# Kernel tuning notes

Hardware: AMD Instinct MI355X
Metric: run time of the kernel (lower is better)

The kernel has to match this reference:

```python
import jax, jax.numpy as jnp
import numpy as np

NUM_HEADS = 8  # config.num_heads


def setup_inputs() -> dict:
    key = jax.random.key(0)
    k0, k1, k2, k3, k4 = jax.random.split(key, 5)
    B, N, C, E = 32, 20000, 8, 512
    query_embeddings = jax.random.normal(k0, (B, E), dtype=jnp.float32)
    all_embeddings = jax.random.normal(k1, (N, E), dtype=jnp.float32)
    label_mask = jax.random.bernoulli(k2, 0.5, (N, C))  # bool multi-label mask
    # per-class MultiheadAttention q/k in-projection params (torch Linear convention: x @ W.T + b)
    Wq = jax.random.normal(k3, (C, E, E), dtype=jnp.float32) * 0.02
    Wk = jax.random.normal(k4, (C, E, E), dtype=jnp.float32) * 0.02
    bq = jnp.zeros((C, E), dtype=jnp.float32)
    bk = jnp.zeros((C, E), dtype=jnp.float32)
    return {
        "query_embeddings": query_embeddings,
        "all_embeddings": all_embeddings,
        "label_mask": label_mask,
        "Wq": Wq,
        "bq": bq,
        "Wk": Wk,
        "bk": bk,
        "n_samples": 5,
    }


def reference(query_embeddings, all_embeddings, label_mask, Wq, bq, Wk, bk, n_samples):
    """Vectorized-over-classes version of EmbeddingSelector.get_similar_samples.

    For each class c: q = query @ Wq[c].T + bq[c]; k_c over the class's database
    members; per-head scaled-dot softmax; attn weights averaged over heads
    (torch MHA need_weights default); top-k over class members. Non-members are
    masked to -inf before softmax, so they get weight 0 and (since every class
    has >> n_samples members) never enter the top-k -- identical math to the
    per-class gather loop, with global indices returned directly.
    """
    C, E, _ = Wq.shape
    H = NUM_HEADS
    dh = E // H
    B = query_embeddings.shape[0]
    N = all_embeddings.shape[0]

    # per-class projections (torch Linear: x @ W.T + b)
    q = jnp.einsum('be,cfe->cbf', query_embeddings, Wq) + bq[:, None, :]   # (C,B,E)
    k = jnp.einsum('ne,cfe->cnf', all_embeddings, Wk) + bk[:, None, :]     # (C,N,E)
    q = q.reshape(C, B, H, dh)
    k = k.reshape(C, N, H, dh)

    scale = 1.0 / jnp.sqrt(jnp.asarray(dh, q.dtype))
    scores = jnp.einsum('cbhd,cnhd->cbhn', q, k) * scale                   # (C,B,H,N)
    member = jnp.transpose(label_mask)[:, None, None, :]                   # (C,1,1,N)
    scores = jnp.where(member, scores, jnp.asarray(-1e9, scores.dtype))
    attn = jax.nn.softmax(scores, axis=-1).mean(axis=2)                    # (C,B,N) head-avg

    weights, indices = jax.lax.top_k(attn, n_samples)                      # (C,B,ns)
    result_weights = jnp.transpose(weights, (1, 0, 2))                     # (B,C,ns)
    result_indices = jnp.transpose(indices, (1, 0, 2)).astype(jnp.int32)   # (B,C,ns) global ids
    return result_indices, result_weights
```

## Files before the change

### kernel.cpp

```cpp
#include <hip/hip_runtime.h>
#include <math.h>

#define B_  32
#define N_  20000
#define C_  8
#define E_  512
#define H_  8
#define SCALE 0.125f
#define UNSC  9.765625e-4f

#define CHUNK 1024
#define NCH   20
#define NC3   157
#define NCG   20
#define SSZ ((size_t)B_ * H_ * N_)

typedef __attribute__((ext_vector_type(8))) _Float16 h8_t;
typedef __attribute__((ext_vector_type(8))) short   s8_t;
typedef __attribute__((ext_vector_type(4))) float f32x4;

#define MFMAH(a, b, c) __builtin_amdgcn_mfma_f32_16x16x32_f16(a, b, c, 0, 0, 0)

#define GLOAD_LDS16(g, l)                                              \
    __builtin_amdgcn_global_load_lds(                                  \
        (const __attribute__((address_space(1))) unsigned int*)(g),    \
        (__attribute__((address_space(3))) unsigned int*)(l), 16, 0, 0)

__device__ inline unsigned short f16_round(float x, float& fv) {
    _Float16 h = (_Float16)x;
    fv = (float)h;
    union { _Float16 hh; unsigned short us; } u;
    u.hh = h;
    return u.us;
}

#define U2P ((size_t)C_ * 16 * 16 * 512)

__global__ __launch_bounds__(256) void k_prep(
        const float* __restrict__ A, short* __restrict__ A2t,
        const float* __restrict__ x, const float* __restrict__ Wq,
        const float* __restrict__ bq, float* __restrict__ q) {
    int bid = blockIdx.x;
    int tid = threadIdx.x;
    if (bid < NC3 * 16) {
        int nc = bid >> 4, ks = bid & 15;
        int n = tid >> 1, kg = (tid & 1) * 2;
        int gn = nc * 128 + n;
        const float* ap = A + (size_t)gn * 512 + ks * 32 + kg * 8;
        s8_t vh[2], vm[2];
        #pragma unroll
        for (int g = 0; g < 2; ++g)
            #pragma unroll
            for (int j = 0; j < 8; ++j) {
                float xv = (gn < N_) ? ap[g * 8 + j] * 32.0f : 0.f;
                float fh, fm;
                vh[g][j] = (short)f16_round(xv, fh);
                vm[g][j] = (short)f16_round(xv - fh, fm);
            }
        short* outp = A2t + ((size_t)nc * 16 + ks) * 8192 + n * 32;
        #pragma unroll
        for (int g = 0; g < 2; ++g) {
            int p = ((kg + g) + (n >> 1)) & 3;
            *(s8_t*)(outp + p * 8)        = vh[g];
            *(s8_t*)(outp + 4096 + p * 8) = vm[g];
        }
    } else {
        int r = bid - NC3 * 16;
        int ft = r & 63, c = r >> 6;
        int f0 = ft * 8;
        __shared__ float wsm[8][66];
        __shared__ float xs[32][66];
        int b = tid & 31, fs = tid >> 5;
        float acc = 0.f;
        const float* W = Wq + (size_t)c * E_ * E_;
        for (int k0 = 0; k0 < E_; k0 += 64) {
            __syncthreads();
            for (int i = tid; i < 512; i += 256)
                wsm[i >> 6][i & 63] = W[(size_t)(f0 + (i >> 6)) * E_ + k0 + (i & 63)];
            for (int i = tid; i < 2048; i += 256)
                xs[i >> 6][i & 63] = x[(size_t)(i >> 6) * E_ + k0 + (i & 63)];
            __syncthreads();
            #pragma unroll
            for (int kk = 0; kk < 64; ++kk)
                acc += xs[b][kk] * wsm[fs][kk];
        }
        q[((size_t)c * B_ + b) * E_ + f0 + fs] = acc + bq[c * E_ + f0 + fs];
    }
}

__global__ __launch_bounds__(256) void k_u2(
        const float* __restrict__ q, const float* __restrict__ Wk,
        const float* __restrict__ bk, short* __restrict__ u2,
        float* __restrict__ qb) {
    int et = blockIdx.x, h = blockIdx.y, c = blockIdx.z;
    int e0 = et * 64;
    __shared__ float qs[32][66];
    __shared__ float wk[64][66];
    int tid = threadIdx.x;
    int b = tid & 31, es = tid >> 5;
    for (int i = tid; i < 2048; i += 256)
        qs[i >> 6][i & 63] = q[((size_t)c * B_ + (i >> 6)) * E_ + h * 64 + (i & 63)];
    const float* W = Wk + (size_t)c * E_ * E_ + (size_t)(h * 64) * E_;
    for (int i = tid; i < 4096; i += 256)
        wk[i >> 6][i & 63] = W[(size_t)(i >> 6) * E_ + e0 + (i & 63)];
    __syncthreads();
    float acc[8] = {};
    for (int d = 0; d < 64; ++d) {
        float qv = qs[b][d];
        #pragma unroll
        for (int j = 0; j < 8; ++j)
            acc[j] += qv * wk[d][es * 8 + j];
    }
    int m   = b * 8 + h;
    int e0s = e0 + es * 8;
    int ks  = e0s >> 5, quad = (e0s & 31) >> 3;
    int lane = (m & 15) + 16 * quad;
    int mt  = m >> 4;
    size_t base = ((((size_t)c * 16 + mt) * 16 + ks) * 512) + (size_t)lane * 8;
    s8_t vh, vm;
    #pragma unroll
    for (int j = 0; j < 8; ++j) {
        float xv = acc[j] * 32.0f, fh, fm;
        vh[j] = (short)f16_round(xv, fh);
        vm[j] = (short)f16_round(xv - fh, fm);
    }
    *(s8_t*)(u2 + base)       = vh;
    *(s8_t*)(u2 + U2P + base) = vm;
    if (et == 0 && es == 0) {
        float s = 0.f;
        const float* bkr = bk + c * E_ + h * 64;
        for (int d = 0; d < 64; ++d) s += qs[b][d] * bkr[d];
        qb[c * 256 + b * 8 + h] = s;
    }
}

__global__ __launch_bounds__(256, 4) void k_scores_mfma(
        const short* __restrict__ u2, const short* __restrict__ A2t,
        const float* __restrict__ qb, const int* __restrict__ mask,
        float* __restrict__ S, float* __restrict__ Zpart, int c0, int CB) {
    __shared__ __align__(16) short As[16384];
    __shared__ float sQb[128];
    __shared__ int   sMask[128];
    int bx = blockIdx.x;
    int x     = bx & 7;
    int rest  = bx >> 3;
    int mh    = rest & 1;
    int rest2 = rest >> 1;
    int z     = rest2 % CB;
    int g     = rest2 / CB;
    int nc    = g * 8 + x;
    if (nc >= NC3) return;
    int c  = c0 + z;
    int tid = threadIdx.x;
    int lane = tid & 63, w = tid >> 6;
    int quad = lane >> 4, l15 = lane & 15;
    int n0 = nc * 128;

    if (tid < 128) {
        sQb[tid] = qb[c * 256 + mh * 128 + tid];
        int n = n0 + tid;
        sMask[tid] = (n < N_) ? mask[(size_t)n * C_ + c] : 0;
    }

    f32x4 acc[2][8];
    #pragma unroll
    for (int i = 0; i < 2; ++i)
        #pragma unroll
        for (int j = 0; j < 8; ++j)
            acc[i][j] = (f32x4){0.f, 0.f, 0.f, 0.f};

    const char* tb = (const char*)A2t + (size_t)nc * 262144;

    for (int ks2 = 0; ks2 < 8; ++ks2) {
        __syncthreads();
        const char* src = tb + (size_t)ks2 * 32768;
        #pragma unroll
        for (int t = 0; t < 8; ++t) {
            int seg = w * 8 + t;
            GLOAD_LDS16(src + (size_t)seg * 1024 + lane * 16,
                        (char*)As + seg * 1024);
        }
        __syncthreads();

        #pragma unroll
        for (int kh = 0; kh < 2; ++kh) {
            int ks = ks2 * 2 + kh;
            const short* Ab = As + kh * 8192;
            h8_t af[2][2];
            #pragma unroll
            for (int mt = 0; mt < 2; ++mt) {
                int mtg = mh * 8 + w * 2 + mt;
                size_t ub = ((((size_t)c * 16 + mtg) * 16 + ks) * 512)
                            + (size_t)lane * 8;
                af[mt][0] = *(const h8_t*)(u2 + ub);
                af[mt][1] = *(const h8_t*)(u2 + U2P + ub);
            }
            #pragma unroll
            for (int half = 0; half < 2; ++half) {
                __builtin_amdgcn_sched_barrier(0);
                #pragma unroll
                for (int q4 = 0; q4 < 4; ++q4) {
                    int nt = half * 4 + q4;
                    int r = nt * 16 + l15;
                    const short* bp = Ab + r * 32 + ((quad + (r >> 1)) & 3) * 8;
                    h8_t b0 = *(const h8_t*)bp;
                    h8_t b1 = *(const h8_t*)(bp + 4096);
                    #pragma unroll
                    for (int mt = 0; mt < 2; ++mt) {
                        f32x4 a = acc[mt][nt];
                        a = MFMAH(af[mt][0], b0, a);
                        a = MFMAH(af[mt][0], b1, a);
                        a = MFMAH(af[mt][1], b0, a);
                        acc[mt][nt] = a;
                    }
                }
            }
        }
    }

    float* Sc = S + (size_t)z * SSZ;
    #pragma unroll
    for (int mt = 0; mt < 2; ++mt) {
        float rs[4] = {0.f, 0.f, 0.f, 0.f};
        #pragma unroll
        for (int nt = 0; nt < 8; ++nt) {
            int nl = nt * 16 + l15;
            int n = n0 + nl;
            int mem = sMask[nl];
            #pragma unroll
            for (int r = 0; r < 4; ++r) {
                int ml = w * 32 + mt * 16 + quad * 4 + r;
                float sc = SCALE * (acc[mt][nt][r] * UNSC + sQb[ml]);
                float ev = mem ? __expf(sc) : 0.f;
                rs[r] += ev;
                if (n < N_) Sc[(size_t)(mh * 128 + ml) * N_ + n] = ev;
            }
        }
        #pragma unroll
        for (int r = 0; r < 4; ++r) {
            float v = rs[r];
            v += __shfl_xor(v, 1); v += __shfl_xor(v, 2);
            v += __shfl_xor(v, 4); v += __shfl_xor(v, 8);
            if (l15 == 0) {
                int ml = w * 32 + mt * 16 + quad * 4 + r;
                Zpart[((size_t)nc * C_ + c) * 256 + mh * 128 + ml] = v;
            }
        }
    }
}

__global__ __launch_bounds__(640) void k_topk(
        const float* __restrict__ S, const float* __restrict__ Zpart,
        float* __restrict__ out, int c0, int ns) {
    int b = blockIdx.x, z = blockIdx.y;
    int c = c0 + z;
    int tid = threadIdx.x;
    int lane = tid & 63, w = tid >> 6;
    const float* Sc = S + (size_t)z * SSZ;

    __shared__ float2 wcand[NCH * 8];

    float zrl;
    {
        int h = lane & 7, sl = lane >> 3;
        const float* zp = Zpart + (size_t)c * 256 + b * 8 + h;
        float s = 0.f;
        for (int nc = sl; nc < NC3; nc += 8)
            s += zp[(size_t)nc * (C_ * 256)];
        s += __shfl_xor(s, 8, 64);
        s += __shfl_xor(s, 16, 64);
        s += __shfl_xor(s, 32, 64);
        zrl = 0.125f / s;
    }
    float zr[H_];
    #pragma unroll
    for (int h = 0; h < H_; ++h) zr[h] = __shfl(zrl, h, 64);

    for (int p = 0; p < 2; ++p) {
        int chunk = w * 2 + p;
        int base = chunk * CHUNK + lane * 4;
        float va[16];
        #pragma unroll
        for (int s = 0; s < 16; ++s) va[s] = 0.f;
        bool ok[4];
        #pragma unroll
        for (int j = 0; j < 4; ++j) ok[j] = (base + j * 256) < N_;

        #pragma unroll
        for (int h = 0; h < H_; ++h) {
            const float* row = Sc + (size_t)(b * H_ + h) * N_;
            float wz = zr[h];
            #pragma unroll
            for (int j = 0; j < 4; ++j) {
                if (ok[j]) {
                    const float4 sv = *(const float4*)&row[base + j * 256];
                    va[j * 4 + 0] += sv.x * wz;
                    va[j * 4 + 1] += sv.y * wz;
                    va[j * 4 + 2] += sv.z * wz;
                    va[j * 4 + 3] += sv.w * wz;
                }
            }
        }
        #pragma unroll
        for (int j = 0; j < 4; ++j)
            if (!ok[j]) {
                va[j * 4 + 0] = -1.f; va[j * 4 + 1] = -1.f;
                va[j * 4 + 2] = -1.f; va[j * 4 + 3] = -1.f;
            }

        for (int j = 0; j < ns; ++j) {
            float bv = va[0]; int bs = 0;
            #pragma unroll
            for (int s = 1; s < 16; ++s)
                if (va[s] > bv) { bv = va[s]; bs = s; }
            int bn = ok[bs >> 2] ? (base + ((bs >> 2) << 8) + (bs & 3)) : N_;
            #pragma unroll
            for (int off = 1; off < 64; off <<= 1) {
                float ov = __shfl_xor(bv, off, 64);
                int   on = __shfl_xor(bn, off, 64);
                if (ov > bv || (ov == bv && on < bn)) { bv = ov; bn = on; }
            }
            if (lane == 0) wcand[chunk * ns + j] = make_float2(bv, (float)bn);
            #pragma unroll
            for (int s = 0; s < 16; ++s) {
                int n_s = base + ((s >> 2) << 8) + (s & 3);
                if (n_s == bn) va[s] = -2.f;
            }
        }
    }
    __syncthreads();

    if (w == 0) {
        int ncand = NCH * ns;
        float v0 = -3.f, v1 = -3.f;
        int   i0 = N_ + 1, i1 = N_ + 2;
        if (lane < ncand)      { float2 e = wcand[lane];      v0 = e.x; i0 = (int)e.y; }
        if (lane + 64 < ncand) { float2 e = wcand[lane + 64]; v1 = e.x; i1 = (int)e.y; }
        for (int j = 0; j < ns; ++j) {
            float bv = v0; int bn = i0;
            if (v1 > bv || (v1 == bv && i1 < bn)) { bv = v1; bn = i1; }
            #pragma unroll
            for (int off = 1; off < 64; off <<= 1) {
                float ov = __shfl_xor(bv, off, 64);
                int   on = __shfl_xor(bn, off, 64);
                if (ov > bv || (ov == bv && on < bn)) { bv = ov; bn = on; }
            }
            if (lane == 0) {
                out[((size_t)b * C_ + c) * ns + j] = (float)bn;
                out[(size_t)B_ * C_ * ns + ((size_t)b * C_ + c) * ns + j] = bv;
            }
            if (i0 == bn) v0 = -3.f;
            if (i1 == bn) v1 = -3.f;
        }
    }
}

extern "C" void kernel_launch(void* const* d_in, const int* in_sizes, int n_in,
                              void* d_out, int out_size, void* d_ws, size_t ws_size,
                              hipStream_t stream) {
    const float* x    = (const float*)d_in[0];
    const float* A    = (const float*)d_in[1];
    const int*   mask = (const int*)  d_in[2];
    const float* Wq   = (const float*)d_in[3];
    const float* bq   = (const float*)d_in[4];
    const float* Wk   = (const float*)d_in[5];
    const float* bk   = (const float*)d_in[6];
    float* out = (float*)d_out;

    int ns = out_size / (2 * B_ * C_);

    float* ws = (float*)d_ws;
    float* q     = ws;
    float* qb    = q     + (size_t)C_ * B_ * E_;
    float* Zpart = qb    + (size_t)C_ * B_ * H_;
    short* u2    = (short*)(Zpart + (size_t)NC3 * C_ * 256);
    short* A2t   = u2 + 2 * U2P;
    float* S     = (float*)(A2t + (size_t)NC3 * 16 * 8192);
    size_t fixedFloats = (size_t)(S - ws);

    int CB = 8;
    while (CB > 1 && (fixedFloats + (size_t)CB * SSZ + 16) * 4 > ws_size)
        CB >>= 1;

    k_prep<<<NC3 * 16 + 512, 256, 0, stream>>>(A, A2t, x, Wq, bq, q);
    k_u2<<<dim3(8, H_, C_), 256, 0, stream>>>(q, Wk, bk, u2, qb);

    for (int c0 = 0; c0 < C_; c0 += CB) {
        k_scores_mfma<<<NCG * 2 * 8 * CB, 256, 0, stream>>>(u2, A2t, qb, mask, S, Zpart, c0, CB);
        k_topk<<<dim3(B_, CB), 640, 0, stream>>>(S, Zpart, out, c0, ns);
    }
}
```

Baseline: 324.7 us.

## Fuse q and u2 projection into prep kernel; halve score tile width

The q projection and the q·Wk fold (u2) now run in 64 per-(class,head) blocks inside the prep kernel, which removes one launch and the q round trip through global memory. Those 64 blocks each do a long serial computation and may sit on the critical path. The scores kernel now splits each 128-row N chunk into two 64-row halves, which doubles the grid, halves LDS per block, and raises the occupancy hint to 6. Zpart gains twice as many partials, and top-k sums them accordingly.

```diff
diff --git a/kernel.cpp b/kernel.cpp
--- a/kernel.cpp
+++ b/kernel.cpp
@@ -39,11 +39,14 @@
 __global__ __launch_bounds__(256) void k_prep(
         const float* __restrict__ A, short* __restrict__ A2t,
         const float* __restrict__ x, const float* __restrict__ Wq,
-        const float* __restrict__ bq, float* __restrict__ q) {
+        const float* __restrict__ bq, const float* __restrict__ Wk,
+        const float* __restrict__ bk, short* __restrict__ u2,
+        float* __restrict__ qb) {
     int bid = blockIdx.x;
     int tid = threadIdx.x;
-    if (bid < NC3 * 16) {
-        int nc = bid >> 4, ks = bid & 15;
+    if (bid >= 64) {
+        int bA = bid - 64;
+        int nc = bA >> 4, ks = bA & 15;
         int n = tid >> 1, kg = (tid & 1) * 2;
         int gn = nc * 128 + n;
         const float* ap = A + (size_t)gn * 512 + ks * 32 + kg * 8;
@@ -65,87 +68,89 @@
             *(s8_t*)(outp + 4096 + p * 8) = vm[g];
         }
     } else {
-        int r = bid - NC3 * 16;
-        int ft = r & 63, c = r >> 6;
-        int f0 = ft * 8;
-        __shared__ float wsm[8][66];
+        int h = bid & 7, c = bid >> 3;
         __shared__ float xs[32][66];
-        int b = tid & 31, fs = tid >> 5;
-        float acc = 0.f;
-        const float* W = Wq + (size_t)c * E_ * E_;
+        __shared__ float wt[64][66];
+        __shared__ float qsl[32][66];
+        int b = tid & 31, grp = tid >> 5;
+
+        float acc8[8] = {};
+        const float* Wqc = Wq + (size_t)c * E_ * E_ + (size_t)(h * 64) * E_;
         for (int k0 = 0; k0 < E_; k0 += 64) {
             __syncthreads();
-            for (int i = tid; i < 512; i += 256)
-                wsm[i >> 6][i & 63] = W[(size_t)(f0 + (i >> 6)) * E_ + k0 + (i & 63)];
             for (int i = tid; i < 2048; i += 256)
                 xs[i >> 6][i & 63] = x[(size_t)(i >> 6) * E_ + k0 + (i & 63)];
+            for (int i = tid; i < 4096; i += 256)
+                wt[i >> 6][i & 63] = Wqc[(size_t)(i >> 6) * E_ + k0 + (i & 63)];
             __syncthreads();
             #pragma unroll
-            for (int kk = 0; kk < 64; ++kk)
-                acc += xs[b][kk] * wsm[fs][kk];
-        }
-        q[((size_t)c * B_ + b) * E_ + f0 + fs] = acc + bq[c * E_ + f0 + fs];
-    }
-}
-
-__global__ __launch_bounds__(256) void k_u2(
-        const float* __restrict__ q, const float* __restrict__ Wk,
-        const float* __restrict__ bk, short* __restrict__ u2,
-        float* __restrict__ qb) {
-    int et = blockIdx.x, h = blockIdx.y, c = blockIdx.z;
-    int e0 = et * 64;
-    __shared__ float qs[32][66];
-    __shared__ float wk[64][66];
-    int tid = threadIdx.x;
-    int b = tid & 31, es = tid >> 5;
-    for (int i = tid; i < 2048; i += 256)
-        qs[i >> 6][i & 63] = q[((size_t)c * B_ + (i >> 6)) * E_ + h * 64 + (i & 63)];
-    const float* W = Wk + (size_t)c * E_ * E_ + (size_t)(h * 64) * E_;
-    for (int i = tid; i < 4096; i += 256)
-        wk[i >> 6][i & 63] = W[(size_t)(i >> 6) * E_ + e0 + (i & 63)];
-    __syncthreads();
-    float acc[8] = {};
-    for (int d = 0; d < 64; ++d) {
-        float qv = qs[b][d];
+            for (int kk = 0; kk < 64; ++kk) {
+                float xv = xs[b][kk];
+                #pragma unroll
+                for (int j = 0; j < 8; ++j)
+                    acc8[j] += xv * wt[grp * 8 + j][kk];
+            }
+        }
+        __syncthreads();
         #pragma unroll
         for (int j = 0; j < 8; ++j)
-            acc[j] += qv * wk[d][es * 8 + j];
-    }
-    int m   = b * 8 + h;
-    int e0s = e0 + es * 8;
-    int ks  = e0s >> 5, quad = (e0s & 31) >> 3;
-    int lane = (m & 15) + 16 * quad;
-    int mt  = m >> 4;
-    size_t base = ((((size_t)c * 16 + mt) * 16 + ks) * 512) + (size_t)lane * 8;
-    s8_t vh, vm;
-    #pragma unroll
-    for (int j = 0; j < 8; ++j) {
-        float xv = acc[j] * 32.0f, fh, fm;
-        vh[j] = (short)f16_round(xv, fh);
-        vm[j] = (short)f16_round(xv - fh, fm);
-    }
-    *(s8_t*)(u2 + base)       = vh;
-    *(s8_t*)(u2 + U2P + base) = vm;
-    if (et == 0 && es == 0) {
-        float s = 0.f;
-        const float* bkr = bk + c * E_ + h * 64;
-        for (int d = 0; d < 64; ++d) s += qs[b][d] * bkr[d];
-        qb[c * 256 + b * 8 + h] = s;
-    }
-}
-
-__global__ __launch_bounds__(256, 4) void k_scores_mfma(
+            qsl[b][grp * 8 + j] = acc8[j] + bq[c * E_ + h * 64 + grp * 8 + j];
+        __syncthreads();
+
+        int es = grp;
+        const float* Wkc = Wk + (size_t)c * E_ * E_ + (size_t)(h * 64) * E_;
+        for (int et = 0; et < 8; ++et) {
+            int e0 = et * 64;
+            __syncthreads();
+            for (int i = tid; i < 4096; i += 256)
+                wt[i >> 6][i & 63] = Wkc[(size_t)(i >> 6) * E_ + e0 + (i & 63)];
+            __syncthreads();
+            float acc[8] = {};
+            for (int d = 0; d < 64; ++d) {
+                float qv = qsl[b][d];
+                #pragma unroll
+                for (int j = 0; j < 8; ++j)
+                    acc[j] += qv * wt[d][es * 8 + j];
+            }
+            int m   = b * 8 + h;
+            int e0s = e0 + es * 8;
+            int ks  = e0s >> 5, quad = (e0s & 31) >> 3;
+            int lane2 = (m & 15) + 16 * quad;
+            int mt  = m >> 4;
+            size_t base = ((((size_t)c * 16 + mt) * 16 + ks) * 512)
+                          + (size_t)lane2 * 8;
+            s8_t vh, vm;
+            #pragma unroll
+            for (int j = 0; j < 8; ++j) {
+                float xv = acc[j] * 32.0f, fh, fm;
+                vh[j] = (short)f16_round(xv, fh);
+                vm[j] = (short)f16_round(xv - fh, fm);
+            }
+            *(s8_t*)(u2 + base)       = vh;
+            *(s8_t*)(u2 + U2P + base) = vm;
+        }
+        if (grp == 0) {
+            float s = 0.f;
+            const float* bkr = bk + c * E_ + h * 64;
+            for (int d = 0; d < 64; ++d) s += qsl[b][d] * bkr[d];
+            qb[c * 256 + b * 8 + h] = s;
+        }
+    }
+}
+
+__global__ __launch_bounds__(256, 6) void k_scores_mfma(
         const short* __restrict__ u2, const short* __restrict__ A2t,
         const float* __restrict__ qb, const int* __restrict__ mask,
         float* __restrict__ S, float* __restrict__ Zpart, int c0, int CB) {
-    __shared__ __align__(16) short As[16384];
+    __shared__ __align__(16) short As[8192];
     __shared__ float sQb[128];
-    __shared__ int   sMask[128];
+    __shared__ int   sMask[64];
     int bx = blockIdx.x;
     int x     = bx & 7;
     int rest  = bx >> 3;
     int mh    = rest & 1;
-    int rest2 = rest >> 1;
+    int nh    = (rest >> 1) & 1;
+    int rest2 = rest >> 2;
     int z     = rest2 % CB;
     int g     = rest2 / CB;
     int nc    = g * 8 + x;
@@ -154,30 +159,31 @@
     int tid = threadIdx.x;
     int lane = tid & 63, w = tid >> 6;
     int quad = lane >> 4, l15 = lane & 15;
-    int n0 = nc * 128;
-
-    if (tid < 128) {
-        sQb[tid] = qb[c * 256 + mh * 128 + tid];
+    int n0 = nc * 128 + nh * 64;
+
+    if (tid < 128) sQb[tid] = qb[c * 256 + mh * 128 + tid];
+    if (tid < 64) {
         int n = n0 + tid;
         sMask[tid] = (n < N_) ? mask[(size_t)n * C_ + c] : 0;
     }
 
-    f32x4 acc[2][8];
+    f32x4 acc[2][4];
     #pragma unroll
     for (int i = 0; i < 2; ++i)
         #pragma unroll
-        for (int j = 0; j < 8; ++j)
+        for (int j = 0; j < 4; ++j)
             acc[i][j] = (f32x4){0.f, 0.f, 0.f, 0.f};
 
-    const char* tb = (const char*)A2t + (size_t)nc * 262144;
+    const char* tb = (const char*)A2t + (size_t)nc * 262144 + nh * 4096;
 
     for (int ks2 = 0; ks2 < 8; ++ks2) {
         __syncthreads();
         const char* src = tb + (size_t)ks2 * 32768;
         #pragma unroll
-        for (int t = 0; t < 8; ++t) {
-            int seg = w * 8 + t;
-            GLOAD_LDS16(src + (size_t)seg * 1024 + lane * 16,
+        for (int t = 0; t < 4; ++t) {
+            int seg = w * 4 + t;
+            int kh = seg >> 3, pl = (seg >> 2) & 1, rg = seg & 3;
+            GLOAD_LDS16(src + kh * 16384 + pl * 8192 + rg * 1024 + lane * 16,
                         (char*)As + seg * 1024);
         }
         __syncthreads();
@@ -185,7 +191,7 @@
         #pragma unroll
         for (int kh = 0; kh < 2; ++kh) {
             int ks = ks2 * 2 + kh;
-            const short* Ab = As + kh * 8192;
+            const short* Ab = As + kh * 4096;
             h8_t af[2][2];
             #pragma unroll
             for (int mt = 0; mt < 2; ++mt) {
@@ -199,12 +205,12 @@
             for (int half = 0; half < 2; ++half) {
                 __builtin_amdgcn_sched_barrier(0);
                 #pragma unroll
-                for (int q4 = 0; q4 < 4; ++q4) {
-                    int nt = half * 4 + q4;
+                for (int q2 = 0; q2 < 2; ++q2) {
+                    int nt = half * 2 + q2;
                     int r = nt * 16 + l15;
                     const short* bp = Ab + r * 32 + ((quad + (r >> 1)) & 3) * 8;
                     h8_t b0 = *(const h8_t*)bp;
-                    h8_t b1 = *(const h8_t*)(bp + 4096);
+                    h8_t b1 = *(const h8_t*)(bp + 2048);
                     #pragma unroll
                     for (int mt = 0; mt < 2; ++mt) {
                         f32x4 a = acc[mt][nt];
@@ -223,7 +229,7 @@
     for (int mt = 0; mt < 2; ++mt) {
         float rs[4] = {0.f, 0.f, 0.f, 0.f};
         #pragma unroll
-        for (int nt = 0; nt < 8; ++nt) {
+        for (int nt = 0; nt < 4; ++nt) {
             int nl = nt * 16 + l15;
             int n = n0 + nl;
             int mem = sMask[nl];
@@ -243,7 +249,7 @@
             v += __shfl_xor(v, 4); v += __shfl_xor(v, 8);
             if (l15 == 0) {
                 int ml = w * 32 + mt * 16 + quad * 4 + r;
-                Zpart[((size_t)nc * C_ + c) * 256 + mh * 128 + ml] = v;
+                Zpart[((size_t)(nc * 2 + nh) * C_ + c) * 256 + mh * 128 + ml] = v;
             }
         }
     }
@@ -265,8 +271,8 @@
         int h = lane & 7, sl = lane >> 3;
         const float* zp = Zpart + (size_t)c * 256 + b * 8 + h;
         float s = 0.f;
-        for (int nc = sl; nc < NC3; nc += 8)
-            s += zp[(size_t)nc * (C_ * 256)];
+        for (int nc2 = sl; nc2 < NC3 * 2; nc2 += 8)
+            s += zp[(size_t)nc2 * (C_ * 256)];
         s += __shfl_xor(s, 8, 64);
         s += __shfl_xor(s, 16, 64);
         s += __shfl_xor(s, 32, 64);
@@ -370,10 +376,9 @@
     int ns = out_size / (2 * B_ * C_);
 
     float* ws = (float*)d_ws;
-    float* q     = ws;
-    float* qb    = q     + (size_t)C_ * B_ * E_;
-    float* Zpart = qb    + (size_t)C_ * B_ * H_;
-    short* u2    = (short*)(Zpart + (size_t)NC3 * C_ * 256);
+    float* qb    = ws;
+    float* Zpart = qb + (size_t)C_ * B_ * H_;
+    short* u2    = (short*)(Zpart + (size_t)NC3 * 2 * C_ * 256);
     short* A2t   = u2 + 2 * U2P;
     float* S     = (float*)(A2t + (size_t)NC3 * 16 * 8192);
     size_t fixedFloats = (size_t)(S - ws);
@@ -382,11 +387,10 @@
     while (CB > 1 && (fixedFloats + (size_t)CB * SSZ + 16) * 4 > ws_size)
         CB >>= 1;
 
-    k_prep<<<NC3 * 16 + 512, 256, 0, stream>>>(A, A2t, x, Wq, bq, q);
-    k_u2<<<dim3(8, H_, C_), 256, 0, stream>>>(q, Wk, bk, u2, qb);
+    k_prep<<<64 + NC3 * 16, 256, 0, stream>>>(A, A2t, x, Wq, bq, Wk, bk, u2, qb);
 
     for (int c0 = 0; c0 < C_; c0 += CB) {
-        k_scores_mfma<<<NCG * 2 * 8 * CB, 256, 0, stream>>>(u2, A2t, qb, mask, S, Zpart, c0, CB);
+        k_scores_mfma<<<NCG * 4 * 8 * CB, 256, 0, stream>>>(u2, A2t, qb, mask, S, Zpart, c0, CB);
         k_topk<<<dim3(B_, CB), 640, 0, stream>>>(S, Zpart, out, c0, ns);
     }
 }
```

Measured after the change: 387.4 us. +19.3%, slower.
